# Performance work log

Hardware: AMD Instinct MI355X
Metric: run time of the kernel (lower is better)

The kernel has to match this reference:

```python
import jax, jax.numpy as jnp
import numpy as np

B, D, K, E = 4096, 2048, 512, 8  # tokens, model dim, kept SVD rank, experts


def setup_inputs() -> dict:
    key = jax.random.key(0)
    ks = jax.random.split(key, 7)
    x = jax.random.normal(ks[0], (B, D), dtype=jnp.float32)
    # frozen base weight (stands in for pretrained_weight)
    W = jax.random.normal(ks[1], (D, D), dtype=jnp.float32) / np.sqrt(D)
    # frozen truncated SVD factors: U_k (D,K) left vecs, V_k (K,D) as sliced in the torch code
    U_k = jnp.linalg.qr(jax.random.normal(ks[2], (D, K), dtype=jnp.float32))[0]
    V_k = jnp.linalg.qr(jax.random.normal(ks[3], (D, K), dtype=jnp.float32))[0].T
    lambda_k = jax.random.normal(ks[4], (E, K), dtype=jnp.float32) * 0.02
    v = jnp.zeros((D,), dtype=jnp.float32)
    router_W1 = jax.random.normal(ks[5], (K, 1), dtype=jnp.float32)
    router_W2 = jax.random.normal(ks[6], (1, E), dtype=jnp.float32)
    return {"x": x, "W": W, "U_k": U_k, "V_k": V_k, "lambda_k": lambda_k,
            "v": v, "router_W1": router_W1, "router_W2": router_W2}


def reference(x, W, U_k, V_k, lambda_k, v, router_W1, router_W2):
    # routing: x @ U_k -> rank-1 router -> softmax over experts
    routing = x @ U_k                                   # (B,K)
    g = jax.nn.softmax((routing @ router_W1) @ router_W2, axis=-1)  # (B,E)
    # per-expert low-rank delta weight, materialized as in the original
    delta_W = jnp.einsum('dk,ek,kn->edn', U_k, lambda_k, V_k)       # (E,D,D)
    W_tot = W[None] + delta_W                           # (E,D,D)
    # F.linear semantics: out = x @ W_tot^T per expert
    expert_out = jnp.einsum('bd,end->ben', x, W_tot)    # (B,E,D)
    out = jnp.einsum('ben,be->bn', expert_out, g)       # gated combine
    return out * (1.0 + v)
```

## Files before the change

kernel.cpp:

```cpp
#include <hip/hip_runtime.h>
#include <hip/hip_bf16.h>
#include <cstdint>

#define B_TOK 4096
#define DDIM  2048
#define KR    512
#define NE    8

using f32x4  = __attribute__((ext_vector_type(4))) float;
using short8 = __attribute__((ext_vector_type(8))) short;
using u16 = unsigned short;

__device__ inline u16 f2bf(float f) {
    union { float f; uint32_t u; } x; x.f = f;
    uint32_t u = x.u;
    return (u16)((u + 0x7fffu + ((u >> 16) & 1u)) >> 16);
}
__device__ inline float bf2f(u16 h) {
    union { uint32_t u; float f; } x; x.u = ((uint32_t)h) << 16;
    return x.f;
}

__device__ inline void gload_lds16(const u16* g, u16* l) {
    __builtin_amdgcn_global_load_lds(
        (const __attribute__((address_space(1))) void*)g,
        (__attribute__((address_space(3))) void*)l, 16, 0, 0);
}

__global__ void cvt_copy2d(const float* __restrict__ src, u16* __restrict__ dst,
                           int rows, int cols4, int src_ld, int dst_ld) {
    int total = rows * cols4;
    for (int i = blockIdx.x * blockDim.x + threadIdx.x; i < total;
         i += gridDim.x * blockDim.x) {
        int r = i / cols4, c = i - r * cols4;
        float4 val = *((const float4*)(src + (size_t)r * src_ld) + c);
        ushort4 o;
        o.x = f2bf(val.x); o.y = f2bf(val.y); o.z = f2bf(val.z); o.w = f2bf(val.w);
        *((ushort4*)(dst + (size_t)r * dst_ld) + c) = o;
    }
}

__global__ __launch_bounds__(64)
void uw1_kernel(const float* __restrict__ U, const float* __restrict__ W1,
                float* __restrict__ u1) {
    int d = blockIdx.x, lane = threadIdx.x;
    const float* row = U + (size_t)d * KR;
    float s = 0.f;
    #pragma unroll
    for (int k = 0; k < KR; k += 64) s += row[k + lane] * W1[k + lane];
    #pragma unroll
    for (int o = 32; o > 0; o >>= 1) s += __shfl_down(s, o);
    if (lane == 0) u1[d] = s;
}

__global__ __launch_bounds__(256)
void router2(const u16* __restrict__ Ax, const float* __restrict__ u1,
             const float* __restrict__ W2, const float* __restrict__ lam,
             const float* __restrict__ tmat, u16* __restrict__ Am) {
    int b = blockIdx.x, tid = threadIdx.x;
    const u16* xr = Ax + (size_t)b * 2560;

    short8 xv = *(const short8*)(xr + tid * 8);
    float4 ua = *((const float4*)(u1 + tid * 8));
    float4 ub = *((const float4*)(u1 + tid * 8) + 1);
    float p = bf2f((u16)xv[0]) * ua.x + bf2f((u16)xv[1]) * ua.y +
              bf2f((u16)xv[2]) * ua.z + bf2f((u16)xv[3]) * ua.w +
              bf2f((u16)xv[4]) * ub.x + bf2f((u16)xv[5]) * ub.y +
              bf2f((u16)xv[6]) * ub.z + bf2f((u16)xv[7]) * ub.w;
    #pragma unroll
    for (int o = 32; o > 0; o >>= 1) p += __shfl_down(p, o);
    __shared__ float sp4[4];
    __shared__ float sbc;
    if ((tid & 63) == 0) sp4[tid >> 6] = p;
    __syncthreads();
    if (tid == 0) sbc = sp4[0] + sp4[1] + sp4[2] + sp4[3];
    __syncthreads();
    float s = sbc;

    float g[NE]; float mx = -1e30f;
    #pragma unroll
    for (int e = 0; e < NE; e++) { g[e] = s * W2[e]; mx = fmaxf(mx, g[e]); }
    float den = 0.f;
    #pragma unroll
    for (int e = 0; e < NE; e++) { g[e] = expf(g[e] - mx); den += g[e]; }
    float inv = 1.0f / den;

    for (int kk = tid; kk < KR; kk += 256) {
        float mu = 0.f;
        #pragma unroll
        for (int e = 0; e < NE; e++) mu += g[e] * lam[e * KR + kk];
        Am[(size_t)b * 2560 + 2048 + kk] =
            f2bf(mu * inv * tmat[(size_t)b * KR + kk]);
    }
}

template<int BM, int BN, int WGM, int WGN, bool HAS_V>
__global__ __launch_bounds__(256, 2)
void gemm_db(const u16* __restrict__ A, const u16* __restrict__ Bm,
             float* __restrict__ C, const float* __restrict__ v,
             int N, int Kc, int lda, int ldb, int nbx) {
    constexpr int MF = BM / (WGM * 16);
    constexpr int NF = BN / (WGN * 16);
    constexpr int ISSA = BM / 32;
    constexpr int ISSB = BN / 32;
    __shared__ u16 sA[2 * BM * 64];
    __shared__ u16 sB[2 * BN * 64];

    const int tid = threadIdx.x;
    const int wid = tid >> 6, lane = tid & 63;
    const int l15 = lane & 15, l4 = lane >> 4;
    const int wm = wid / WGN, wn = wid % WGN;

    const int nwg = gridDim.x;
    const int id = (blockIdx.x & 7) * (nwg >> 3) + (blockIdx.x >> 3);
    const int row0 = (id / nbx) * BM;
    const int col0 = (id % nbx) * BN;

    const int srow = tid >> 3;
    const int scol = ((tid & 7) ^ (srow & 7)) << 3;
    const u16* gA = A + (size_t)(row0 + srow) * lda + scol;
    const u16* gB = Bm + (size_t)(col0 + srow) * ldb + scol;

    f32x4 acc[MF][NF] = {};
    const int nt = Kc >> 6;

    #pragma unroll
    for (int i = 0; i < ISSA; i++)
        gload_lds16(gA + (size_t)i * 32 * lda, sA + i * 2048 + wid * 512);
    #pragma unroll
    for (int i = 0; i < ISSB; i++)
        gload_lds16(gB + (size_t)i * 32 * ldb, sB + i * 2048 + wid * 512);
    __syncthreads();

    for (int t = 0; t < nt; ++t) {
        const int cur = t & 1;
        if (t + 1 < nt) {
            const int nxt = cur ^ 1;
            const u16* gAk = gA + (size_t)(t + 1) * 64;
            const u16* gBk = gB + (size_t)(t + 1) * 64;
            #pragma unroll
            for (int i = 0; i < ISSA; i++)
                gload_lds16(gAk + (size_t)i * 32 * lda,
                            sA + nxt * BM * 64 + i * 2048 + wid * 512);
            #pragma unroll
            for (int i = 0; i < ISSB; i++)
                gload_lds16(gBk + (size_t)i * 32 * ldb,
                            sB + nxt * BN * 64 + i * 2048 + wid * 512);
        }
        const u16* a0 = sA + cur * BM * 64;
        const u16* b0 = sB + cur * BN * 64;
        #pragma unroll
        for (int kc = 0; kc < 8; kc += 4) {
            short8 af[MF], bv[NF];
            #pragma unroll
            for (int mf = 0; mf < MF; mf++) {
                int row = wm * MF * 16 + mf * 16 + l15;
                int ch = (kc + l4) ^ (row & 7);
                af[mf] = *(const short8*)(a0 + row * 64 + ch * 8);
            }
            #pragma unroll
            for (int nf = 0; nf < NF; nf++) {
                int row = wn * NF * 16 + nf * 16 + l15;
                int ch = (kc + l4) ^ (row & 7);
                bv[nf] = *(const short8*)(b0 + row * 64 + ch * 8);
            }
            #pragma unroll
            for (int mf = 0; mf < MF; mf++)
                #pragma unroll
                for (int nf = 0; nf < NF; nf++)
                    acc[mf][nf] = __builtin_amdgcn_mfma_f32_16x16x32_bf16(
                        af[mf], bv[nf], acc[mf][nf], 0, 0, 0);
        }
        __syncthreads();
    }

    #pragma unroll
    for (int nf = 0; nf < NF; nf++) {
        int col = col0 + wn * NF * 16 + nf * 16 + l15;
        float sc = HAS_V ? (1.0f + v[col]) : 1.0f;
        #pragma unroll
        for (int mf = 0; mf < MF; mf++) {
            int row = row0 + wm * MF * 16 + mf * 16 + l4 * 4;
            #pragma unroll
            for (int r2 = 0; r2 < 4; r2++)
                C[(size_t)(row + r2) * N + col] = acc[mf][nf][r2] * sc;
        }
    }
}

template<int BM, int BN, int WGM, int WGN, bool HAS_V>
__global__ __launch_bounds__(WGM * WGN * 64, 1)
void gemm_ring(const u16* __restrict__ A, const u16* __restrict__ Bm,
               float* __restrict__ C, const float* __restrict__ v,
               int N, int Kc, int lda, int ldb, int nbx) {
    constexpr int NT = WGM * WGN * 64;
    constexpr int MF = BM / (WGM * 16);
    constexpr int NF = BN / (WGN * 16);
    constexpr int SLOT = (BM + BN) * 64;
    constexpr int ROWS = NT / 8;
    constexpr int ISSA = BM / ROWS;
    constexpr int ISSB = BN / ROWS;
    static_assert(ISSA + ISSB == 6, "vmcnt literals assume 6 loads/tile");
    __shared__ u16 lds[3 * SLOT];

    const int tid = threadIdx.x;
    const int wid = tid >> 6, lane = tid & 63;
    const int l15 = lane & 15, l4 = lane >> 4;
    const int wm = wid / WGN, wn = wid % WGN;

    const int nwg = gridDim.x;
    const int id = (blockIdx.x & 7) * (nwg >> 3) + (blockIdx.x >> 3);
    const int row0 = (id / nbx) * BM;
    const int col0 = (id % nbx) * BN;

    const int srow = tid >> 3;
    const int scol = ((tid & 7) ^ (srow & 7)) << 3;
    const u16* gA = A + (size_t)(row0 + srow) * lda + scol;
    const u16* gB = Bm + (size_t)(col0 + srow) * ldb + scol;

    f32x4 acc[MF][NF] = {};
    const int nt = Kc >> 6;

    #pragma unroll
    for (int p = 0; p < 2; p++) {
        const u16* gAt = gA + p * 64;
        const u16* gBt = gB + p * 64;
        u16* sl = lds + p * SLOT;
        #pragma unroll
        for (int i = 0; i < ISSA; i++)
            gload_lds16(gAt + (size_t)i * ROWS * lda,
                        sl + i * ROWS * 64 + wid * 512);
        #pragma unroll
        for (int i = 0; i < ISSB; i++)
            gload_lds16(gBt + (size_t)i * ROWS * ldb,
                        sl + BM * 64 + i * ROWS * 64 + wid * 512);
    }
    asm volatile("s_waitcnt vmcnt(6)" ::: "memory");
    __builtin_amdgcn_s_barrier();
    asm volatile("" ::: "memory");

    int sc = 0, sp = 2;
    for (int t = 0; t < nt; ++t) {
        if (t + 2 < nt) {
            const u16* gAt = gA + (size_t)(t + 2) * 64;
            const u16* gBt = gB + (size_t)(t + 2) * 64;
            u16* sl = lds + sp * SLOT;
            #pragma unroll
            for (int i = 0; i < ISSA; i++)
                gload_lds16(gAt + (size_t)i * ROWS * lda,
                            sl + i * ROWS * 64 + wid * 512);
            #pragma unroll
            for (int i = 0; i < ISSB; i++)
                gload_lds16(gBt + (size_t)i * ROWS * ldb,
                            sl + BM * 64 + i * ROWS * 64 + wid * 512);
        }
        const u16* a0 = lds + sc * SLOT;
        const u16* b0 = a0 + BM * 64;
        __builtin_amdgcn_s_setprio(1);
        #pragma unroll
        for (int kc = 0; kc < 8; kc += 4) {
            short8 af[MF], bv[NF];
            #pragma unroll
            for (int mf = 0; mf < MF; mf++) {
                int row = wm * MF * 16 + mf * 16 + l15;
                int ch = (kc + l4) ^ (row & 7);
                af[mf] = *(const short8*)(a0 + row * 64 + ch * 8);
            }
            #pragma unroll
            for (int nf = 0; nf < NF; nf++) {
                int row = wn * NF * 16 + nf * 16 + l15;
                int ch = (kc + l4) ^ (row & 7);
                bv[nf] = *(const short8*)(b0 + row * 64 + ch * 8);
            }
            #pragma unroll
            for (int mf = 0; mf < MF; mf++)
                #pragma unroll
                for (int nf = 0; nf < NF; nf++)
                    acc[mf][nf] = __builtin_amdgcn_mfma_f32_16x16x32_bf16(
                        af[mf], bv[nf], acc[mf][nf], 0, 0, 0);
        }
        __builtin_amdgcn_s_setprio(0);

        const int rem = nt - 1 - t;
        if (rem == 0) break;
        if (rem >= 2) asm volatile("s_waitcnt vmcnt(6)" ::: "memory");
        else          asm volatile("s_waitcnt vmcnt(0)" ::: "memory");
        __builtin_amdgcn_s_barrier();
        asm volatile("" ::: "memory");
        sc = (sc == 2) ? 0 : sc + 1;
        sp = (sp == 2) ? 0 : sp + 1;
    }

    #pragma unroll
    for (int nf = 0; nf < NF; nf++) {
        int col = col0 + wn * NF * 16 + nf * 16 + l15;
        float sc2 = HAS_V ? (1.0f + v[col]) : 1.0f;
        #pragma unroll
        for (int mf = 0; mf < MF; mf++) {
            int row = row0 + wm * MF * 16 + mf * 16 + l4 * 4;
            #pragma unroll
            for (int r2 = 0; r2 < 4; r2++)
                C[(size_t)(row + r2) * N + col] = acc[mf][nf][r2] * sc2;
        }
    }
}

extern "C" void kernel_launch(void* const* d_in, const int* in_sizes, int n_in,
                              void* d_out, int out_size, void* d_ws, size_t ws_size,
                              hipStream_t stream) {
    const float* x   = (const float*)d_in[0];
    const float* W   = (const float*)d_in[1];
    const float* U   = (const float*)d_in[2];
    const float* V   = (const float*)d_in[3];
    const float* lam = (const float*)d_in[4];
    const float* v   = (const float*)d_in[5];
    const float* W1  = (const float*)d_in[6];
    const float* W2  = (const float*)d_in[7];
    float* out = (float*)d_out;

    char* ws = (char*)d_ws;
    u16*   Aaug = (u16*)ws;
    u16*   BigB = (u16*)(ws + 20971520);
    u16*   Vb   = (u16*)(ws + 31457280);
    float* tmat = (float*)(ws + 33554432);
    float* u1   = (float*)(ws + 41943040);

    cvt_copy2d<<<2048, 256, 0, stream>>>(x, Aaug, 4096, 512, 2048, 2560);
    cvt_copy2d<<<2048, 256, 0, stream>>>(W, BigB, 2048, 512, 2048, 2560);
    cvt_copy2d<<<1024, 256, 0, stream>>>(U, BigB + 2048, 2048, 128, 512, 2560);
    cvt_copy2d<<<1024, 256, 0, stream>>>(V, Vb, 512, 512, 2048, 2048);
    uw1_kernel<<<2048, 64, 0, stream>>>(U, W1, u1);

    gemm_db<128, 64, 4, 1, false><<<256, 256, 0, stream>>>(
        Aaug, Vb, tmat, nullptr, 512, 2048, 2560, 2048, 8);

    router2<<<4096, 256, 0, stream>>>(Aaug, u1, W2, lam, tmat, Aaug);

    gemm_ring<256, 128, 4, 2, true><<<256, 512, 0, stream>>>(
        Aaug, BigB, out, v, 2048, 2560, 2560, 2560, 16);
}
```

Baseline: 106.4 us.

## Fuse prep kernels into one launch and split GEMM k-loop into interleaved phases

Merges the four fp32-to-bf16 conversion launches and the U·W1 reduction into a single prep kernel, removing launch overhead and tail gaps between small kernels. Rewrites the main GEMM loop into two half-tile phases. Each phase issues its LDS fragment reads, then half of the next tile's global-to-LDS loads, then barriers and runs the MFMAs, so loads and math from different waves interleave. This adds extra barriers per tile, which could cost more than the overlap saves.

```diff
diff --git a/kernel.cpp b/kernel.cpp
--- a/kernel.cpp
+++ b/kernel.cpp
@@ -27,30 +27,48 @@
         (__attribute__((address_space(3))) void*)l, 16, 0, 0);
 }
 
-__global__ void cvt_copy2d(const float* __restrict__ src, u16* __restrict__ dst,
-                           int rows, int cols4, int src_ld, int dst_ld) {
-    int total = rows * cols4;
-    for (int i = blockIdx.x * blockDim.x + threadIdx.x; i < total;
-         i += gridDim.x * blockDim.x) {
-        int r = i / cols4, c = i - r * cols4;
-        float4 val = *((const float4*)(src + (size_t)r * src_ld) + c);
-        ushort4 o;
-        o.x = f2bf(val.x); o.y = f2bf(val.y); o.z = f2bf(val.z); o.w = f2bf(val.w);
-        *((ushort4*)(dst + (size_t)r * dst_ld) + c) = o;
-    }
-}
-
-__global__ __launch_bounds__(64)
-void uw1_kernel(const float* __restrict__ U, const float* __restrict__ W1,
-                float* __restrict__ u1) {
-    int d = blockIdx.x, lane = threadIdx.x;
-    const float* row = U + (size_t)d * KR;
-    float s = 0.f;
-    #pragma unroll
-    for (int k = 0; k < KR; k += 64) s += row[k + lane] * W1[k + lane];
-    #pragma unroll
-    for (int o = 32; o > 0; o >>= 1) s += __shfl_down(s, o);
-    if (lane == 0) u1[d] = s;
+template<int COLS4, int SRC_LD, int DST_LD>
+__device__ inline void cvt_region(const float* __restrict__ src,
+                                  u16* __restrict__ dst, int i) {
+    int r = i / COLS4, c = i - r * COLS4;
+    float4 val = *((const float4*)(src + (size_t)r * SRC_LD) + c);
+    ushort4 o;
+    o.x = f2bf(val.x); o.y = f2bf(val.y); o.z = f2bf(val.z); o.w = f2bf(val.w);
+    *(ushort4*)(dst + (size_t)r * DST_LD + c * 4) = o;
+}
+
+__global__ __launch_bounds__(256)
+void prep_all(const float* __restrict__ x, const float* __restrict__ W,
+              const float* __restrict__ U, const float* __restrict__ V,
+              const float* __restrict__ W1,
+              u16* __restrict__ Aaug, u16* __restrict__ BigB,
+              u16* __restrict__ Vb, float* __restrict__ u1) {
+    constexpr int NB_COPY = 1792;
+    constexpr int N_X = 4096 * 512;
+    constexpr int N_W = 2048 * 512;
+    constexpr int N_U = 2048 * 128;
+    constexpr int N_V = 512 * 512;
+    constexpr int N_TOT = N_X + N_W + N_U + N_V;
+    int b = blockIdx.x;
+    if (b < NB_COPY) {
+        for (int i = b * 256 + threadIdx.x; i < N_TOT; i += NB_COPY * 256) {
+            if (i < N_X)                cvt_region<512, 2048, 2560>(x, Aaug, i);
+            else if (i < N_X + N_W)     cvt_region<512, 2048, 2560>(W, BigB, i - N_X);
+            else if (i < N_X + N_W + N_U)
+                cvt_region<128, 512, 2560>(U, BigB + 2048, i - N_X - N_W);
+            else                        cvt_region<512, 2048, 2048>(V, Vb, i - N_X - N_W - N_U);
+        }
+    } else {
+        int wrow = (b - NB_COPY) * 4 + (threadIdx.x >> 6);
+        int lane = threadIdx.x & 63;
+        const float* row = U + (size_t)wrow * KR;
+        float s = 0.f;
+        #pragma unroll
+        for (int k = 0; k < KR; k += 64) s += row[k + lane] * W1[k + lane];
+        #pragma unroll
+        for (int o = 32; o > 0; o >>= 1) s += __shfl_down(s, o);
+        if (lane == 0) u1[wrow] = s;
+    }
 }
 
 __global__ __launch_bounds__(256)
@@ -190,9 +208,9 @@
 
 template<int BM, int BN, int WGM, int WGN, bool HAS_V>
 __global__ __launch_bounds__(WGM * WGN * 64, 1)
-void gemm_ring(const u16* __restrict__ A, const u16* __restrict__ Bm,
-               float* __restrict__ C, const float* __restrict__ v,
-               int N, int Kc, int lda, int ldb, int nbx) {
+void gemm_ph(const u16* __restrict__ A, const u16* __restrict__ Bm,
+             float* __restrict__ C, const float* __restrict__ v,
+             int N, int Kc, int lda, int ldb, int nbx) {
     constexpr int NT = WGM * WGN * 64;
     constexpr int MF = BM / (WGM * 16);
     constexpr int NF = BN / (WGN * 16);
@@ -237,48 +255,72 @@
     }
     asm volatile("s_waitcnt vmcnt(6)" ::: "memory");
     __builtin_amdgcn_s_barrier();
-    asm volatile("" ::: "memory");
 
     int sc = 0, sp = 2;
     for (int t = 0; t < nt; ++t) {
-        if (t + 2 < nt) {
-            const u16* gAt = gA + (size_t)(t + 2) * 64;
-            const u16* gBt = gB + (size_t)(t + 2) * 64;
-            u16* sl = lds + sp * SLOT;
-            #pragma unroll
-            for (int i = 0; i < ISSA; i++)
-                gload_lds16(gAt + (size_t)i * ROWS * lda,
-                            sl + i * ROWS * 64 + wid * 512);
-            #pragma unroll
-            for (int i = 0; i < ISSB; i++)
-                gload_lds16(gBt + (size_t)i * ROWS * ldb,
-                            sl + BM * 64 + i * ROWS * 64 + wid * 512);
-        }
         const u16* a0 = lds + sc * SLOT;
         const u16* b0 = a0 + BM * 64;
+        const u16* gAt = gA + (size_t)(t + 2) * 64;
+        const u16* gBt = gB + (size_t)(t + 2) * 64;
+        u16* sl = lds + sp * SLOT;
+        const bool pf = (t + 2 < nt);
+
+        short8 af[MF], bv[NF];
+        #pragma unroll
+        for (int mf = 0; mf < MF; mf++) {
+            int row = wm * MF * 16 + mf * 16 + l15;
+            int ch = l4 ^ (row & 7);
+            af[mf] = *(const short8*)(a0 + row * 64 + ch * 8);
+        }
+        #pragma unroll
+        for (int nf = 0; nf < NF; nf++) {
+            int row = wn * NF * 16 + nf * 16 + l15;
+            int ch = l4 ^ (row & 7);
+            bv[nf] = *(const short8*)(b0 + row * 64 + ch * 8);
+        }
+        if (pf) {
+            gload_lds16(gAt,                         sl + wid * 512);
+            gload_lds16(gAt + (size_t)ROWS * lda,    sl + ROWS * 64 + wid * 512);
+            gload_lds16(gAt + (size_t)2 * ROWS * lda, sl + 2 * ROWS * 64 + wid * 512);
+        }
+        __builtin_amdgcn_s_barrier();
+        asm volatile("s_waitcnt lgkmcnt(0)" ::: "memory");
         __builtin_amdgcn_s_setprio(1);
         #pragma unroll
-        for (int kc = 0; kc < 8; kc += 4) {
-            short8 af[MF], bv[NF];
-            #pragma unroll
-            for (int mf = 0; mf < MF; mf++) {
-                int row = wm * MF * 16 + mf * 16 + l15;
-                int ch = (kc + l4) ^ (row & 7);
-                af[mf] = *(const short8*)(a0 + row * 64 + ch * 8);
-            }
-            #pragma unroll
-            for (int nf = 0; nf < NF; nf++) {
-                int row = wn * NF * 16 + nf * 16 + l15;
-                int ch = (kc + l4) ^ (row & 7);
-                bv[nf] = *(const short8*)(b0 + row * 64 + ch * 8);
-            }
-            #pragma unroll
-            for (int mf = 0; mf < MF; mf++)
-                #pragma unroll
-                for (int nf = 0; nf < NF; nf++)
-                    acc[mf][nf] = __builtin_amdgcn_mfma_f32_16x16x32_bf16(
-                        af[mf], bv[nf], acc[mf][nf], 0, 0, 0);
-        }
+        for (int mf = 0; mf < MF; mf++)
+            #pragma unroll
+            for (int nf = 0; nf < NF; nf++)
+                acc[mf][nf] = __builtin_amdgcn_mfma_f32_16x16x32_bf16(
+                    af[mf], bv[nf], acc[mf][nf], 0, 0, 0);
+        __builtin_amdgcn_s_setprio(0);
+        __builtin_amdgcn_s_barrier();
+
+        #pragma unroll
+        for (int mf = 0; mf < MF; mf++) {
+            int row = wm * MF * 16 + mf * 16 + l15;
+            int ch = (4 + l4) ^ (row & 7);
+            af[mf] = *(const short8*)(a0 + row * 64 + ch * 8);
+        }
+        #pragma unroll
+        for (int nf = 0; nf < NF; nf++) {
+            int row = wn * NF * 16 + nf * 16 + l15;
+            int ch = (4 + l4) ^ (row & 7);
+            bv[nf] = *(const short8*)(b0 + row * 64 + ch * 8);
+        }
+        if (pf) {
+            gload_lds16(gAt + (size_t)3 * ROWS * lda, sl + 3 * ROWS * 64 + wid * 512);
+            gload_lds16(gBt,                          sl + BM * 64 + wid * 512);
+            gload_lds16(gBt + (size_t)ROWS * ldb,     sl + BM * 64 + ROWS * 64 + wid * 512);
+        }
+        __builtin_amdgcn_s_barrier();
+        asm volatile("s_waitcnt lgkmcnt(0)" ::: "memory");
+        __builtin_amdgcn_s_setprio(1);
+        #pragma unroll
+        for (int mf = 0; mf < MF; mf++)
+            #pragma unroll
+            for (int nf = 0; nf < NF; nf++)
+                acc[mf][nf] = __builtin_amdgcn_mfma_f32_16x16x32_bf16(
+                    af[mf], bv[nf], acc[mf][nf], 0, 0, 0);
         __builtin_amdgcn_s_setprio(0);
 
         const int rem = nt - 1 - t;
@@ -286,7 +328,6 @@
         if (rem >= 2) asm volatile("s_waitcnt vmcnt(6)" ::: "memory");
         else          asm volatile("s_waitcnt vmcnt(0)" ::: "memory");
         __builtin_amdgcn_s_barrier();
-        asm volatile("" ::: "memory");
         sc = (sc == 2) ? 0 : sc + 1;
         sp = (sp == 2) ? 0 : sp + 1;
     }
@@ -325,17 +366,13 @@
     float* tmat = (float*)(ws + 33554432);
     float* u1   = (float*)(ws + 41943040);
 
-    cvt_copy2d<<<2048, 256, 0, stream>>>(x, Aaug, 4096, 512, 2048, 2560);
-    cvt_copy2d<<<2048, 256, 0, stream>>>(W, BigB, 2048, 512, 2048, 2560);
-    cvt_copy2d<<<1024, 256, 0, stream>>>(U, BigB + 2048, 2048, 128, 512, 2560);
-    cvt_copy2d<<<1024, 256, 0, stream>>>(V, Vb, 512, 512, 2048, 2048);
-    uw1_kernel<<<2048, 64, 0, stream>>>(U, W1, u1);
+    prep_all<<<2304, 256, 0, stream>>>(x, W, U, V, W1, Aaug, BigB, Vb, u1);
 
     gemm_db<128, 64, 4, 1, false><<<256, 256, 0, stream>>>(
         Aaug, Vb, tmat, nullptr, 512, 2048, 2560, 2048, 8);
 
     router2<<<4096, 256, 0, stream>>>(Aaug, u1, W2, lam, tmat, Aaug);
 
-    gemm_ring<256, 128, 4, 2, true><<<256, 512, 0, stream>>>(
+    gemm_ph<256, 128, 4, 2, true><<<256, 512, 0, stream>>>(
         Aaug, BigB, out, v, 2048, 2560, 2560, 2560, 16);
 }
```

Result: faster. 101.9 us (-4.3%).

## Fuse prep kernels, fold router dot into projection GEMM, bf16 intermediate, XCD tile mapping

Applied to the files above, without the earlier changes.

Merges the four conversion kernels and the U·W1 reduction into one prep_all launch. The router's per-token x·u1 dot product becomes an extra row of the V projection matrix, so the first GEMM computes it as column 512 of a 576-wide output, and the router kernel no longer needs its block reduction or x read. The intermediate t matrix is stored in bf16 instead of fp32 to halve its traffic. The main GEMM gets a region-based block-to-XCD mapping so tiles sharing A/B rows stay on the same XCD's L2. Rounding the router logit through bf16 adds some precision risk, and the first GEMM does 12.5% more padded work.

```diff
diff --git a/kernel.cpp b/kernel.cpp
--- a/kernel.cpp
+++ b/kernel.cpp
@@ -27,55 +27,63 @@
         (__attribute__((address_space(3))) void*)l, 16, 0, 0);
 }
 
-__global__ void cvt_copy2d(const float* __restrict__ src, u16* __restrict__ dst,
-                           int rows, int cols4, int src_ld, int dst_ld) {
-    int total = rows * cols4;
-    for (int i = blockIdx.x * blockDim.x + threadIdx.x; i < total;
-         i += gridDim.x * blockDim.x) {
-        int r = i / cols4, c = i - r * cols4;
-        float4 val = *((const float4*)(src + (size_t)r * src_ld) + c);
-        ushort4 o;
-        o.x = f2bf(val.x); o.y = f2bf(val.y); o.z = f2bf(val.z); o.w = f2bf(val.w);
-        *((ushort4*)(dst + (size_t)r * dst_ld) + c) = o;
-    }
-}
-
-__global__ __launch_bounds__(64)
-void uw1_kernel(const float* __restrict__ U, const float* __restrict__ W1,
-                float* __restrict__ u1) {
-    int d = blockIdx.x, lane = threadIdx.x;
-    const float* row = U + (size_t)d * KR;
-    float s = 0.f;
-    #pragma unroll
-    for (int k = 0; k < KR; k += 64) s += row[k + lane] * W1[k + lane];
-    #pragma unroll
-    for (int o = 32; o > 0; o >>= 1) s += __shfl_down(s, o);
-    if (lane == 0) u1[d] = s;
+template<int COLS4, int SRC_LD, int DST_LD>
+__device__ inline void cvt_region(const float* __restrict__ src,
+                                  u16* __restrict__ dst, int i) {
+    int r = i / COLS4, c = i - r * COLS4;
+    float4 val = *((const float4*)(src + (size_t)r * SRC_LD) + c);
+    ushort4 o;
+    o.x = f2bf(val.x); o.y = f2bf(val.y); o.z = f2bf(val.z); o.w = f2bf(val.w);
+    *(ushort4*)(dst + (size_t)r * DST_LD + c * 4) = o;
 }
 
 __global__ __launch_bounds__(256)
-void router2(const u16* __restrict__ Ax, const float* __restrict__ u1,
-             const float* __restrict__ W2, const float* __restrict__ lam,
-             const float* __restrict__ tmat, u16* __restrict__ Am) {
-    int b = blockIdx.x, tid = threadIdx.x;
-    const u16* xr = Ax + (size_t)b * 2560;
-
-    short8 xv = *(const short8*)(xr + tid * 8);
-    float4 ua = *((const float4*)(u1 + tid * 8));
-    float4 ub = *((const float4*)(u1 + tid * 8) + 1);
-    float p = bf2f((u16)xv[0]) * ua.x + bf2f((u16)xv[1]) * ua.y +
-              bf2f((u16)xv[2]) * ua.z + bf2f((u16)xv[3]) * ua.w +
-              bf2f((u16)xv[4]) * ub.x + bf2f((u16)xv[5]) * ub.y +
-              bf2f((u16)xv[6]) * ub.z + bf2f((u16)xv[7]) * ub.w;
-    #pragma unroll
-    for (int o = 32; o > 0; o >>= 1) p += __shfl_down(p, o);
-    __shared__ float sp4[4];
-    __shared__ float sbc;
-    if ((tid & 63) == 0) sp4[tid >> 6] = p;
-    __syncthreads();
-    if (tid == 0) sbc = sp4[0] + sp4[1] + sp4[2] + sp4[3];
-    __syncthreads();
-    float s = sbc;
+void prep_all(const float* __restrict__ x, const float* __restrict__ W,
+              const float* __restrict__ U, const float* __restrict__ V,
+              const float* __restrict__ W1,
+              u16* __restrict__ Aaug, u16* __restrict__ BigB,
+              u16* __restrict__ Vb) {
+    constexpr int NB_COPY = 1792;
+    constexpr int N_X = 4096 * 512;
+    constexpr int N_W = 2048 * 512;
+    constexpr int N_U = 2048 * 128;
+    constexpr int N_V = 512 * 512;
+    constexpr int N_Z = 63 * 512;
+    constexpr int N_TOT = N_X + N_W + N_U + N_V + N_Z;
+    int b = blockIdx.x;
+    if (b < NB_COPY) {
+        for (int i = b * 256 + threadIdx.x; i < N_TOT; i += NB_COPY * 256) {
+            if (i < N_X)                cvt_region<512, 2048, 2560>(x, Aaug, i);
+            else if (i < N_X + N_W)     cvt_region<512, 2048, 2560>(W, BigB, i - N_X);
+            else if (i < N_X + N_W + N_U)
+                cvt_region<128, 512, 2560>(U, BigB + 2048, i - N_X - N_W);
+            else if (i < N_X + N_W + N_U + N_V)
+                cvt_region<512, 2048, 2048>(V, Vb, i - N_X - N_W - N_U);
+            else {
+                int z = i - (N_X + N_W + N_U + N_V);
+                ushort4 zz; zz.x = 0; zz.y = 0; zz.z = 0; zz.w = 0;
+                *(ushort4*)(Vb + (size_t)513 * 2048 + (size_t)z * 4) = zz;
+            }
+        }
+    } else {
+        int wrow = (b - NB_COPY) * 4 + (threadIdx.x >> 6);
+        int lane = threadIdx.x & 63;
+        const float* row = U + (size_t)wrow * KR;
+        float s = 0.f;
+        #pragma unroll
+        for (int k = 0; k < KR; k += 64) s += row[k + lane] * W1[k + lane];
+        #pragma unroll
+        for (int o = 32; o > 0; o >>= 1) s += __shfl_down(s, o);
+        if (lane == 0) Vb[(size_t)512 * 2048 + wrow] = f2bf(s);
+    }
+}
+
+__global__ __launch_bounds__(256)
+void router3(const u16* __restrict__ tb, const float* __restrict__ W2,
+             const float* __restrict__ lam, u16* __restrict__ Am) {
+    int row = blockIdx.x, tid = threadIdx.x;
+    const u16* tr = tb + (size_t)row * 576;
+    float s = bf2f(tr[512]);
 
     float g[NE]; float mx = -1e30f;
     #pragma unroll
@@ -85,19 +93,19 @@
     for (int e = 0; e < NE; e++) { g[e] = expf(g[e] - mx); den += g[e]; }
     float inv = 1.0f / den;
 
+    #pragma unroll
     for (int kk = tid; kk < KR; kk += 256) {
         float mu = 0.f;
         #pragma unroll
         for (int e = 0; e < NE; e++) mu += g[e] * lam[e * KR + kk];
-        Am[(size_t)b * 2560 + 2048 + kk] =
-            f2bf(mu * inv * tmat[(size_t)b * KR + kk]);
-    }
-}
-
-template<int BM, int BN, int WGM, int WGN, bool HAS_V>
+        Am[(size_t)row * 2560 + 2048 + kk] = f2bf(mu * inv * bf2f(tr[kk]));
+    }
+}
+
+template<int BM, int BN, int WGM, int WGN, bool HAS_V, bool OUT_BF16>
 __global__ __launch_bounds__(256, 2)
 void gemm_db(const u16* __restrict__ A, const u16* __restrict__ Bm,
-             float* __restrict__ C, const float* __restrict__ v,
+             void* __restrict__ Cv, const float* __restrict__ v,
              int N, int Kc, int lda, int ldb, int nbx) {
     constexpr int MF = BM / (WGM * 16);
     constexpr int NF = BN / (WGN * 16);
@@ -182,25 +190,27 @@
         for (int mf = 0; mf < MF; mf++) {
             int row = row0 + wm * MF * 16 + mf * 16 + l4 * 4;
             #pragma unroll
-            for (int r2 = 0; r2 < 4; r2++)
-                C[(size_t)(row + r2) * N + col] = acc[mf][nf][r2] * sc;
-        }
-    }
-}
-
-template<int BM, int BN, int WGM, int WGN, bool HAS_V>
-__global__ __launch_bounds__(WGM * WGN * 64, 1)
+            for (int r2 = 0; r2 < 4; r2++) {
+                float val = acc[mf][nf][r2] * sc;
+                if constexpr (OUT_BF16)
+                    ((u16*)Cv)[(size_t)(row + r2) * N + col] = f2bf(val);
+                else
+                    ((float*)Cv)[(size_t)(row + r2) * N + col] = val;
+            }
+        }
+    }
+}
+
+template<bool HAS_V, bool REGION>
+__global__ __launch_bounds__(512, 1)
 void gemm_ring(const u16* __restrict__ A, const u16* __restrict__ Bm,
                float* __restrict__ C, const float* __restrict__ v,
                int N, int Kc, int lda, int ldb, int nbx) {
-    constexpr int NT = WGM * WGN * 64;
-    constexpr int MF = BM / (WGM * 16);
-    constexpr int NF = BN / (WGN * 16);
+    constexpr int BM = 256, BN = 128, WGN = 2;
+    constexpr int MF = 4, NF = 4;
     constexpr int SLOT = (BM + BN) * 64;
-    constexpr int ROWS = NT / 8;
-    constexpr int ISSA = BM / ROWS;
-    constexpr int ISSB = BN / ROWS;
-    static_assert(ISSA + ISSB == 6, "vmcnt literals assume 6 loads/tile");
+    constexpr int ROWS = 64;
+    constexpr int ISSA = 4, ISSB = 2;
     __shared__ u16 lds[3 * SLOT];
 
     const int tid = threadIdx.x;
@@ -208,10 +218,18 @@
     const int l15 = lane & 15, l4 = lane >> 4;
     const int wm = wid / WGN, wn = wid % WGN;
 
-    const int nwg = gridDim.x;
-    const int id = (blockIdx.x & 7) * (nwg >> 3) + (blockIdx.x >> 3);
-    const int row0 = (id / nbx) * BM;
-    const int col0 = (id % nbx) * BN;
+    int row0, col0;
+    if (REGION) {
+        const int xcd = blockIdx.x & 7;
+        const int j = blockIdx.x >> 3;
+        row0 = ((xcd >> 1) * 4 + (j >> 3)) * BM;
+        col0 = ((xcd & 1) * 8 + (j & 7)) * BN;
+    } else {
+        const int nwg = gridDim.x;
+        const int id = (blockIdx.x & 7) * (nwg >> 3) + (blockIdx.x >> 3);
+        row0 = (id / nbx) * BM;
+        col0 = (id % nbx) * BN;
+    }
 
     const int srow = tid >> 3;
     const int scol = ((tid & 7) ^ (srow & 7)) << 3;
@@ -319,23 +337,18 @@
     float* out = (float*)d_out;
 
     char* ws = (char*)d_ws;
-    u16*   Aaug = (u16*)ws;
-    u16*   BigB = (u16*)(ws + 20971520);
-    u16*   Vb   = (u16*)(ws + 31457280);
-    float* tmat = (float*)(ws + 33554432);
-    float* u1   = (float*)(ws + 41943040);
-
-    cvt_copy2d<<<2048, 256, 0, stream>>>(x, Aaug, 4096, 512, 2048, 2560);
-    cvt_copy2d<<<2048, 256, 0, stream>>>(W, BigB, 2048, 512, 2048, 2560);
-    cvt_copy2d<<<1024, 256, 0, stream>>>(U, BigB + 2048, 2048, 128, 512, 2560);
-    cvt_copy2d<<<1024, 256, 0, stream>>>(V, Vb, 512, 512, 2048, 2048);
-    uw1_kernel<<<2048, 64, 0, stream>>>(U, W1, u1);
-
-    gemm_db<128, 64, 4, 1, false><<<256, 256, 0, stream>>>(
-        Aaug, Vb, tmat, nullptr, 512, 2048, 2560, 2048, 8);
-
-    router2<<<4096, 256, 0, stream>>>(Aaug, u1, W2, lam, tmat, Aaug);
-
-    gemm_ring<256, 128, 4, 2, true><<<256, 512, 0, stream>>>(
+    u16* Aaug  = (u16*)ws;
+    u16* BigB  = (u16*)(ws + 20971520);
+    u16* Vb    = (u16*)(ws + 31457280);
+    u16* tmatb = (u16*)(ws + 33816576);
+
+    prep_all<<<2304, 256, 0, stream>>>(x, W, U, V, W1, Aaug, BigB, Vb);
+
+    gemm_db<128, 64, 4, 1, false, true><<<288, 256, 0, stream>>>(
+        Aaug, Vb, tmatb, nullptr, 576, 2048, 2560, 2048, 9);
+
+    router3<<<4096, 256, 0, stream>>>(tmatb, W2, lam, Aaug);
+
+    gemm_ring<true, true><<<256, 512, 0, stream>>>(
         Aaug, BigB, out, v, 2048, 2560, 2560, 2560, 16);
 }
```

Measured after the change: 99.55 us. 1.07x faster.
